# Optimization experiments

Hardware: AMD Instinct MI355X
Metric: run time of the kernel (lower is better)

Reference implementation:

```python
import jax, jax.numpy as jnp
import numpy as np

N_NODES = 100000
N_EDGES = 1600000
IN_CH = 512
HID_CH = 256
OUT_CH = 32
K = 10


def setup_inputs() -> dict:
    key = jax.random.key(0)
    k_x, k_e, k_w1, k_b1, k_w2, k_b2 = jax.random.split(key, 6)
    x = jax.random.normal(k_x, (N_NODES, IN_CH), dtype=jnp.float32)
    edge_index = jax.random.randint(k_e, (2, N_EDGES), 0, N_NODES, dtype=jnp.int64)
    s1 = 1.0 / np.sqrt(IN_CH)
    s2 = 1.0 / np.sqrt(HID_CH)
    W1 = jax.random.uniform(k_w1, (IN_CH, HID_CH), jnp.float32, -s1, s1)
    b1 = jax.random.uniform(k_b1, (HID_CH,), jnp.float32, -s1, s1)
    W2 = jax.random.uniform(k_w2, (HID_CH, OUT_CH), jnp.float32, -s2, s2)
    b2 = jax.random.uniform(k_b2, (OUT_CH,), jnp.float32, -s2, s2)
    gamma = jnp.ones((K + 1,), jnp.float32) / (K + 1)
    return {"x": x, "edge_index": edge_index, "W1": W1, "b1": b1,
            "W2": W2, "b2": b2, "gamma": gamma}


def reference(x, edge_index, W1, b1, W2, b2, gamma):
    # MLP (dropout is identity in eval mode)
    h = jax.nn.relu(x @ W1 + b1) @ W2 + b2  # [N, out]
    row, col = edge_index[0], edge_index[1]
    # symmetric normalization: deg over destination nodes (col)
    deg = jax.ops.segment_sum(jnp.ones((N_EDGES,), h.dtype), col,
                              num_segments=N_NODES)
    deg_inv_sqrt = jnp.where(deg > 0, jax.lax.rsqrt(jnp.maximum(deg, 1.0)), 0.0)
    norm = (deg_inv_sqrt[row] * deg_inv_sqrt[col])[:, None]  # [E, 1]
    out = gamma[0] * h
    h_k = h
    for k in range(1, K + 1):
        # one hop: gather source feats, scale, scatter-add to destinations
        h_k = jax.ops.segment_sum(norm * h_k[row], col, num_segments=N_NODES)
        out = out + gamma[k] * h_k
    return out
```

## Files before the change

### kernel.cpp

```cpp
#include <hip/hip_runtime.h>
#include <hip/hip_bf16.h>

#define NN    100000
#define NE    1600000
#define INCH  512
#define HIDCH 256
#define OUTCH 32
#define KHOPS 10
#define NEPAD (NE + 3 * NN)
#define NBKT  8
#define BDIV  12500
#define BCAP  204800
#define EPB_A 8192
#define EPB_B 2048

typedef __attribute__((ext_vector_type(8))) short short8;
typedef __attribute__((ext_vector_type(4))) float f32x4;

#define GLOAD_LDS16(gsrc, ldst) \
  __builtin_amdgcn_global_load_lds((const __attribute__((address_space(1))) void*)(gsrc), \
                                   (__attribute__((address_space(3))) void*)(ldst), 16, 0, 0)

constexpr size_t ws_align(size_t x) { return (x + 255) & ~(size_t)255; }
constexpr size_t USZ = ws_align((size_t)(NN + 1) * 32 * 2);
constexpr size_t USH = USZ / 2;
constexpr size_t OFF_H1    = 0;
constexpr size_t OFF_U0    = OFF_H1    + ws_align((size_t)NN*HIDCH*2);
constexpr size_t OFF_W1TH  = OFF_U0    + 11 * USZ;
constexpr size_t OFF_W1TL  = OFF_W1TH  + ws_align((size_t)HIDCH*INCH*2);
constexpr size_t OFF_W2TH  = OFF_W1TL  + ws_align((size_t)HIDCH*INCH*2);
constexpr size_t OFF_W2TL  = OFF_W2TH  + ws_align((size_t)OUTCH*HIDCH*2);
constexpr size_t OFF_DEG   = OFF_W2TL  + ws_align((size_t)OUTCH*HIDCH*2);
constexpr size_t OFF_DIS   = OFF_DEG   + ws_align((size_t)NN*4);
constexpr size_t OFF_RP    = OFF_DIS   + ws_align((size_t)NN*4);
constexpr size_t OFF_CUR   = OFF_RP    + ws_align((size_t)(NN+1)*4);
constexpr size_t OFF_NAP   = OFF_CUR   + ws_align((size_t)NN*4);
constexpr size_t OFF_POSV  = OFF_NAP   + ws_align((size_t)NN*4);
constexpr size_t OFF_PDGP  = OFF_POSV  + ws_align((size_t)NN*4);
constexpr size_t OFF_D2P   = OFF_PDGP  + ws_align((size_t)NN*4);
constexpr size_t OFF_DSQP  = OFF_D2P   + ws_align((size_t)NN*4);
constexpr size_t OFF_CSR   = OFF_DSQP  + ws_align((size_t)NN*4);
constexpr size_t OFF_PART  = OFF_CSR   + ws_align((size_t)NEPAD*4);
constexpr size_t OFF_OFFS  = OFF_PART  + ws_align(512);
constexpr size_t OFF_BCNT  = OFF_OFFS  + ws_align(512);
constexpr size_t OFF_BINH  = OFF_BCNT  + ws_align(32);
constexpr size_t OFF_BINO  = OFF_BINH  + ws_align(256);
constexpr size_t OFF_BINC  = OFF_BINO  + ws_align(256);
constexpr size_t OFF_EPK8  = OFF_BINC  + ws_align(256);

__device__ __forceinline__ unsigned short bf16_rne(float f) {
  unsigned int u = __float_as_uint(f);
  u += 0x7fffu + ((u >> 16) & 1u);
  return (unsigned short)(u >> 16);
}
__device__ __forceinline__ float bf16_to_f32(unsigned short h) {
  return __uint_as_float(((unsigned int)h) << 16);
}
__device__ __forceinline__ float bflo(unsigned int w) {
  return __uint_as_float(w << 16);
}
__device__ __forceinline__ float bfhi(unsigned int w) {
  return __uint_as_float(w & 0xffff0000u);
}

__global__ __launch_bounds__(256) void k_bucket(const int* __restrict__ ei,
                                                int* __restrict__ deg,
                                                int* __restrict__ bcnt,
                                                int2* __restrict__ epk8) {
  __shared__ int hist[NBKT], rbase[NBKT], lcur[NBKT];
  const int t = threadIdx.x;
  const int e0 = blockIdx.x * EPB_A;
  if (t < NBKT) hist[t] = 0;
  __syncthreads();
  for (int i = t; i < EPB_A; i += 256) {
    int e = e0 + i;
    if (e < NE) {
      int c = ei[NE + e];
      atomicAdd(&deg[c], 1);
      atomicAdd(&hist[c / BDIV], 1);
    }
  }
  __syncthreads();
  if (t < NBKT) {
    rbase[t] = atomicAdd(&bcnt[t], hist[t]);
    lcur[t] = 0;
  }
  __syncthreads();
  for (int i = t; i < EPB_A; i += 256) {
    int e = e0 + i;
    if (e < NE) {
      int r = ei[e], c = ei[NE + e];
      int b = c / BDIV;
      int slot = atomicAdd(&lcur[b], 1);
      epk8[(size_t)b * BCAP + rbase[b] + slot] = make_int2(r, c);
    }
  }
}

__global__ __launch_bounds__(256) void k_dis(const int* __restrict__ deg,
                                             float* __restrict__ dis,
                                             unsigned short* __restrict__ u0) {
  int v = blockIdx.x * 256 + threadIdx.x;
  if (v < NN) {
    int d = deg[v];
    dis[v] = d > 0 ? rsqrtf((float)d) : 0.0f;
  }
  if (blockIdx.x == 0 && threadIdx.x < 160) {
    int tab = threadIdx.x >> 4, li = threadIdx.x & 15;
    ((unsigned int*)(u0 + (size_t)tab * USH))[(size_t)NN * 16 + li] = 0;
  }
}

__global__ __launch_bounds__(256) void k_hist(const int* __restrict__ deg,
                                              int* __restrict__ binh) {
  __shared__ int h[64];
  const int t = threadIdx.x;
  if (t < 64) h[t] = 0;
  __syncthreads();
  int v = blockIdx.x * 256 + t;
  if (v < NN) {
    int bin = ((deg[v] + 3) & ~3) >> 2;
    if (bin > 63) bin = 63;
    atomicAdd(&h[bin], 1);
  }
  __syncthreads();
  if (t < 64 && h[t]) atomicAdd(&binh[t], h[t]);
}

__global__ __launch_bounds__(64) void k_binscan(const int* __restrict__ binh,
                                                int* __restrict__ bino,
                                                int* __restrict__ binc) {
  __shared__ int s[64];
  int t = threadIdx.x;
  int v = binh[t];
  s[t] = v;
  __syncthreads();
  for (int d = 1; d < 64; d <<= 1) {
    int x = (t >= d) ? s[t - d] : 0;
    __syncthreads();
    s[t] += x;
    __syncthreads();
  }
  bino[t] = s[t] - v;
  binc[t] = s[t] - v;
}

__global__ __launch_bounds__(256) void k_place(const int* __restrict__ deg,
                                               int* __restrict__ binc,
                                               int* __restrict__ nap,
                                               int* __restrict__ posv,
                                               int* __restrict__ pdgp) {
  __shared__ int h[64], rb[64], lc[64];
  const int t = threadIdx.x;
  if (t < 64) h[t] = 0;
  __syncthreads();
  int v = blockIdx.x * 256 + t;
  int pdeg = 0, bin = 0;
  bool valid = v < NN;
  if (valid) {
    pdeg = (deg[v] + 3) & ~3;
    bin = pdeg >> 2;
    if (bin > 63) bin = 63;
    atomicAdd(&h[bin], 1);
  }
  __syncthreads();
  if (t < 64) {
    rb[t] = h[t] ? atomicAdd(&binc[t], h[t]) : 0;
    lc[t] = 0;
  }
  __syncthreads();
  if (valid) {
    int slot = atomicAdd(&lc[bin], 1);
    int pos = rb[bin] + slot;
    nap[pos] = v;
    posv[v] = pos;
    pdgp[pos] = pdeg;
  }
}

__global__ __launch_bounds__(256) void k_scan1(const int* __restrict__ pdgp,
                                               int* __restrict__ rp,
                                               int* __restrict__ part) {
  __shared__ int s[256];
  int b = blockIdx.x, t = threadIdx.x;
  int base = b * 1024 + t * 4;
  int v0 = (base + 0 < NN) ? pdgp[base + 0] : 0;
  int v1 = (base + 1 < NN) ? pdgp[base + 1] : 0;
  int v2 = (base + 2 < NN) ? pdgp[base + 2] : 0;
  int v3 = (base + 3 < NN) ? pdgp[base + 3] : 0;
  int tot = v0 + v1 + v2 + v3;
  s[t] = tot;
  __syncthreads();
  for (int d = 1; d < 256; d <<= 1) {
    int x = (t >= d) ? s[t - d] : 0;
    __syncthreads();
    s[t] += x;
    __syncthreads();
  }
  int excl = s[t] - tot;
  if (t == 255) part[b] = s[255];
  if (base + 0 < NN) rp[base + 0] = excl;
  if (base + 1 < NN) rp[base + 1] = excl + v0;
  if (base + 2 < NN) rp[base + 2] = excl + v0 + v1;
  if (base + 3 < NN) rp[base + 3] = excl + v0 + v1 + v2;
}

__global__ __launch_bounds__(128) void k_scan2(const int* __restrict__ part,
                                               int* __restrict__ offs) {
  __shared__ int s[128];
  int t = threadIdx.x;
  int v = (t < 98) ? part[t] : 0;
  s[t] = v;
  __syncthreads();
  for (int d = 1; d < 128; d <<= 1) {
    int x = (t >= d) ? s[t - d] : 0;
    __syncthreads();
    s[t] += x;
    __syncthreads();
  }
  if (t < 98) offs[t] = s[t] - v;
}

__global__ __launch_bounds__(256) void k_scan3(int* __restrict__ rp,
                                               const int* __restrict__ offs,
                                               const int* __restrict__ part) {
  int b = blockIdx.x, t = threadIdx.x;
  int o = offs[b];
  int base = b * 1024 + t * 4;
#pragma unroll
  for (int j = 0; j < 4; ++j) {
    int i = base + j;
    if (i < NN) rp[i] += o;
  }
  if (b == 0 && t == 0) rp[NN] = offs[97] + part[97];
}

__global__ __launch_bounds__(256) void k_curinit(const int* __restrict__ nap,
                                                 const int* __restrict__ rp,
                                                 const int* __restrict__ deg,
                                                 const float* __restrict__ dis,
                                                 int* __restrict__ cur,
                                                 float* __restrict__ d2p,
                                                 float* __restrict__ dsqp) {
  int p = blockIdx.x * 256 + threadIdx.x;
  if (p < NN) {
    int v = nap[p];
    cur[v] = rp[p];
    float dv = dis[v];
    d2p[p] = dv * dv;
    int d = deg[v];
    dsqp[p] = d > 0 ? sqrtf((float)d) : 0.0f;
  }
}

__global__ __launch_bounds__(256) void k_fill2(const int2* __restrict__ epk8,
                                               const int* __restrict__ bcnt,
                                               const int* __restrict__ posv,
                                               int* __restrict__ cur,
                                               int* __restrict__ csrc) {
  const int bucket = blockIdx.x & 7;
  const int chunk = blockIdx.x >> 3;
  const int cnt = bcnt[bucket];
  const int lo = chunk * EPB_B;
  int n = cnt - lo;
  if (n > EPB_B) n = EPB_B;
  const int2* src = epk8 + (size_t)bucket * BCAP + lo;
  for (int i = threadIdx.x; i < n; i += 256) {
    int2 rc = src[i];
    int p = atomicAdd(&cur[rc.y], 1);
    csrc[p] = posv[rc.x];
  }
}

__global__ __launch_bounds__(256) void k_pad(const int* __restrict__ nap,
                                             const int* __restrict__ cur,
                                             const int* __restrict__ rp,
                                             int* __restrict__ csrc) {
  int p = blockIdx.x * 256 + threadIdx.x;
  if (p < NN) {
    int v = nap[p];
    int q = cur[v], e = rp[p + 1];
    for (; q < e; ++q) csrc[q] = NN;
  }
}

__global__ __launch_bounds__(256) void k_splitT(const float* __restrict__ src,
                                                unsigned short* __restrict__ dh,
                                                unsigned short* __restrict__ dl,
                                                int K, int N) {
  int idx = blockIdx.x * 256 + threadIdx.x;
  if (idx >= K * N) return;
  int n = idx / K, k = idx - n * K;
  float v = src[(size_t)k * N + n];
  unsigned short h = bf16_rne(v);
  dh[idx] = h;
  dl[idx] = bf16_rne(v - bf16_to_f32(h));
}

__global__ __launch_bounds__(512, 2) void k_gemm1(const float* __restrict__ X,
                                                  const unsigned short* __restrict__ W1Th,
                                                  const float* __restrict__ bias1,
                                                  unsigned short* __restrict__ H1bf) {
  __shared__ __align__(16) unsigned short Ah[2][4096];
  __shared__ __align__(16) unsigned short Bh[2][8192];
  const int t = threadIdx.x;
  const int m0 = blockIdx.x * 128;
  const int w = t >> 6, lane = t & 63;
  const int wm = w >> 2, wn = w & 3;

  const int arow = t >> 2;
  const int achk = t & 3;
  int axrow = m0 + arow; if (axrow >= NN) axrow = NN - 1;
  const float* aptr = X + (size_t)axrow * INCH + achk * 8;
  int aidx = (arow >> 4) * 512 + ((arow & 15) + achk * 16) * 8;
  aidx ^= ((aidx >> 7) & 3) << 4;
  const int aroff = (lane * 8) ^ (((lane >> 4) & 3) << 4);

  const int bn0 = (w * 16) + (lane & 15);
  const int bko = (lane >> 4) * 8;
  const unsigned short* bs0 = W1Th + (size_t)bn0 * INCH + bko;
  const unsigned short* bs1 = W1Th + (size_t)(bn0 + 128) * INCH + bko;

  f32x4 acc[4][4] = {};
  float4 av0, av1;

  av0 = *(const float4*)(aptr);
  av1 = *(const float4*)(aptr + 4);
  GLOAD_LDS16(bs0, &Bh[0][w * 512]);
  GLOAD_LDS16(bs1, &Bh[0][(w + 8) * 512]);
  {
    float af[8] = {av0.x, av0.y, av0.z, av0.w, av1.x, av1.y, av1.z, av1.w};
    short8 ah;
#pragma unroll
    for (int i = 0; i < 8; ++i) {
      unsigned int u = __float_as_uint(af[i]);
      ah[i] = (short)((u + 0x7fffu + ((u >> 16) & 1u)) >> 16);
    }
    *(short8*)&Ah[0][aidx] = ah;
  }
  __syncthreads();

#pragma unroll
  for (int it = 0; it < 16; ++it) {
    const int cur = it & 1, nxt = cur ^ 1;
    const int k0 = it * 32;
    if (it < 15) {
      av0 = *(const float4*)(aptr + k0 + 32);
      av1 = *(const float4*)(aptr + k0 + 36);
      GLOAD_LDS16(bs0 + k0 + 32, &Bh[nxt][w * 512]);
      GLOAD_LDS16(bs1 + k0 + 32, &Bh[nxt][(w + 8) * 512]);
    }
    short8 afrag[4];
#pragma unroll
    for (int mf = 0; mf < 4; ++mf)
      afrag[mf] = *(const short8*)&Ah[cur][(wm * 4 + mf) * 512 + aroff];
#pragma unroll
    for (int nf = 0; nf < 4; ++nf) {
      short8 bfh = *(const short8*)&Bh[cur][(wn * 4 + nf) * 512 + lane * 8];
#pragma unroll
      for (int mf = 0; mf < 4; ++mf) {
        acc[mf][nf] = __builtin_amdgcn_mfma_f32_16x16x32_bf16(afrag[mf], bfh, acc[mf][nf], 0, 0, 0);
      }
    }
    if (it < 15) {
      float af[8] = {av0.x, av0.y, av0.z, av0.w, av1.x, av1.y, av1.z, av1.w};
      short8 ah;
#pragma unroll
      for (int i = 0; i < 8; ++i) {
        unsigned int u = __float_as_uint(af[i]);
        ah[i] = (short)((u + 0x7fffu + ((u >> 16) & 1u)) >> 16);
      }
      *(short8*)&Ah[nxt][aidx] = ah;
    }
    __syncthreads();
  }

  const int colbase = wn * 64 + (lane & 15);
  const int rowbase = m0 + wm * 64 + ((lane >> 4) << 2);
#pragma unroll
  for (int nf = 0; nf < 4; ++nf) {
    int col = colbase + nf * 16;
    float b = bias1[col];
#pragma unroll
    for (int mf = 0; mf < 4; ++mf) {
#pragma unroll
      for (int r = 0; r < 4; ++r) {
        int row = rowbase + mf * 16 + r;
        if (row < NN) {
          float h = fmaxf(acc[mf][nf][r] + b, 0.f);
          H1bf[(size_t)row * HIDCH + col] = bf16_rne(h);
        }
      }
    }
  }
}

__global__ __launch_bounds__(256) void k_gemm2(const unsigned short* __restrict__ H1bf,
                                               const unsigned short* __restrict__ W2Th,
                                               const unsigned short* __restrict__ W2Tl,
                                               const float* __restrict__ bias2,
                                               const float* __restrict__ gamma,
                                               const float* __restrict__ dis,
                                               const int* __restrict__ posv,
                                               unsigned short* __restrict__ u0,
                                               float* __restrict__ out) {
  __shared__ __align__(16) unsigned short A2[8192];
  __shared__ __align__(16) unsigned short B2h[2048], B2l[2048];
  const int t = threadIdx.x;
  const int m0 = blockIdx.x * 128;

  const int arow = t >> 1;
  int axrow = m0 + arow; if (axrow >= NN) axrow = NN - 1;
  const int akb = (t & 1) * 32;
  const unsigned short* ap = H1bf + (size_t)axrow * HIDCH + akb;
  const int abase = ((arow >> 4) * 2 + (akb >> 5)) * 512 + (arow & 15) * 8;

  const int bnr = t >> 3, bkq = (t & 7) * 8;
  const int bslot = ((bnr >> 4) * 2 + (bkq >> 5)) * 512 +
                    ((bnr & 15) + (((bkq & 31) >> 3) << 4)) * 8;
  const unsigned short* bhp = W2Th + (size_t)bnr * HIDCH + bkq;
  const unsigned short* blp = W2Tl + (size_t)bnr * HIDCH + bkq;

  const int w = t >> 6, lane = t & 63;

  f32x4 acc[2][2] = {};

  for (int k0 = 0; k0 < HIDCH; k0 += 64) {
    uint4 a0 = *(const uint4*)(ap + k0);
    uint4 a1 = *(const uint4*)(ap + k0 + 8);
    uint4 a2 = *(const uint4*)(ap + k0 + 16);
    uint4 a3 = *(const uint4*)(ap + k0 + 24);
    uint4 bh = *(const uint4*)(bhp + k0);
    uint4 bl = *(const uint4*)(blp + k0);

    __syncthreads();

    *(uint4*)&A2[abase + 0 * 128] = a0;
    *(uint4*)&A2[abase + 1 * 128] = a1;
    *(uint4*)&A2[abase + 2 * 128] = a2;
    *(uint4*)&A2[abase + 3 * 128] = a3;
    *(uint4*)&B2h[bslot] = bh;
    *(uint4*)&B2l[bslot] = bl;

    __syncthreads();

    const short8* AV  = (const short8*)A2;
    const short8* BHV = (const short8*)B2h;
    const short8* BLV = (const short8*)B2l;
#pragma unroll
    for (int k32 = 0; k32 < 2; ++k32) {
      short8 bfh[2], bfl[2];
#pragma unroll
      for (int nf = 0; nf < 2; ++nf) {
        bfh[nf] = BHV[(nf * 2 + k32) * 64 + lane];
        bfl[nf] = BLV[(nf * 2 + k32) * 64 + lane];
      }
#pragma unroll
      for (int mf = 0; mf < 2; ++mf) {
        short8 a = AV[((w * 2 + mf) * 2 + k32) * 64 + lane];
#pragma unroll
        for (int nf = 0; nf < 2; ++nf) {
          acc[mf][nf] = __builtin_amdgcn_mfma_f32_16x16x32_bf16(a, bfh[nf], acc[mf][nf], 0, 0, 0);
          acc[mf][nf] = __builtin_amdgcn_mfma_f32_16x16x32_bf16(a, bfl[nf], acc[mf][nf], 0, 0, 0);
        }
      }
    }
  }

  const float g0 = gamma[0];
  const int colb = lane & 15;
  const int rowb = m0 + w * 32 + ((lane >> 4) << 2);
  const float b2c0 = bias2[colb], b2c1 = bias2[16 + colb];
#pragma unroll
  for (int mf = 0; mf < 2; ++mf) {
#pragma unroll
    for (int r = 0; r < 4; ++r) {
      int row = rowb + mf * 16 + r;
      if (row < NN) {
        float dv = dis[row];
        float h0 = acc[mf][0][r] + b2c0;
        float h1 = acc[mf][1][r] + b2c1;
        size_t op = (size_t)posv[row] * 32 + colb;
        u0[op] = bf16_rne(dv * h0);
        u0[op + 16] = bf16_rne(dv * h1);
        size_t o = (size_t)row * 32 + colb;
        out[o] = g0 * h0;
        out[o + 16] = g0 * h1;
      }
    }
  }
}

__global__ __launch_bounds__(256) void k_hop(const unsigned short* __restrict__ Uin,
                                             unsigned short* __restrict__ Uout,
                                             const int* __restrict__ rp,
                                             const int* __restrict__ csrc,
                                             const float* __restrict__ d2p) {
  const int t = threadIdx.x;
  const int g = t >> 4;
  const int li = t & 15;
  const int p = blockIdx.x * 16 + g;
  const int s = rp[p], e = rp[p + 1];
  const unsigned int* Uin32 = (const unsigned int*)Uin;

  float ax0 = 0.f, ay0 = 0.f, ax1 = 0.f, ay1 = 0.f;
  float ax2 = 0.f, ay2 = 0.f, ax3 = 0.f, ay3 = 0.f;
  int j = s;
  for (; j + 8 <= e; j += 8) {
    int4 sa = *(const int4*)&csrc[j];
    int4 sb = *(const int4*)&csrc[j + 4];
    unsigned int w0 = Uin32[(size_t)sa.x * 16 + li];
    unsigned int w1 = Uin32[(size_t)sa.y * 16 + li];
    unsigned int w2 = Uin32[(size_t)sa.z * 16 + li];
    unsigned int w3 = Uin32[(size_t)sa.w * 16 + li];
    unsigned int w4 = Uin32[(size_t)sb.x * 16 + li];
    unsigned int w5 = Uin32[(size_t)sb.y * 16 + li];
    unsigned int w6 = Uin32[(size_t)sb.z * 16 + li];
    unsigned int w7 = Uin32[(size_t)sb.w * 16 + li];
    ax0 += bflo(w0); ay0 += bfhi(w0);
    ax1 += bflo(w1); ay1 += bfhi(w1);
    ax2 += bflo(w2); ay2 += bfhi(w2);
    ax3 += bflo(w3); ay3 += bfhi(w3);
    ax0 += bflo(w4); ay0 += bfhi(w4);
    ax1 += bflo(w5); ay1 += bfhi(w5);
    ax2 += bflo(w6); ay2 += bfhi(w6);
    ax3 += bflo(w7); ay3 += bfhi(w7);
  }
  if (j < e) {
    int4 sa = *(const int4*)&csrc[j];
    unsigned int w0 = Uin32[(size_t)sa.x * 16 + li];
    unsigned int w1 = Uin32[(size_t)sa.y * 16 + li];
    unsigned int w2 = Uin32[(size_t)sa.z * 16 + li];
    unsigned int w3 = Uin32[(size_t)sa.w * 16 + li];
    ax0 += bflo(w0); ay0 += bfhi(w0);
    ax1 += bflo(w1); ay1 += bfhi(w1);
    ax2 += bflo(w2); ay2 += bfhi(w2);
    ax3 += bflo(w3); ay3 += bfhi(w3);
  }
  const float Sx = (ax0 + ax1) + (ax2 + ax3);
  const float Sy = (ay0 + ay1) + (ay2 + ay3);
  const float d2 = d2p[p];
  unsigned int packed = (unsigned int)bf16_rne(d2 * Sx) |
                        ((unsigned int)bf16_rne(d2 * Sy) << 16);
  ((unsigned int*)Uout)[(size_t)p * 16 + li] = packed;
}

__global__ __launch_bounds__(256) void k_merge(const unsigned short* __restrict__ u1,
                                               const int* __restrict__ nap,
                                               const float* __restrict__ dsqp,
                                               const float* __restrict__ gamma,
                                               float* __restrict__ out) {
  const int idx = blockIdx.x * 256 + threadIdx.x;
  const int p = idx >> 4;
  const int li = idx & 15;
  const int v = nap[p];
  const float f = dsqp[p];
  const size_t o = (size_t)v * 32 + li * 2;
  float2 acc = *(const float2*)&out[o];
#pragma unroll
  for (int k = 0; k < KHOPS; ++k) {
    unsigned int w = ((const unsigned int*)(u1 + (size_t)k * USH))[(size_t)p * 16 + li];
    float gk = gamma[k + 1] * f;
    acc.x = fmaf(gk, bflo(w), acc.x);
    acc.y = fmaf(gk, bfhi(w), acc.y);
  }
  *(float2*)&out[o] = acc;
}

extern "C" void kernel_launch(void* const* d_in, const int* in_sizes, int n_in,
                              void* d_out, int out_size, void* d_ws, size_t ws_size,
                              hipStream_t stream) {
  const float* x     = (const float*)d_in[0];
  const int*   ei    = (const int*)d_in[1];
  const float* W1    = (const float*)d_in[2];
  const float* b1    = (const float*)d_in[3];
  const float* W2    = (const float*)d_in[4];
  const float* b2    = (const float*)d_in[5];
  const float* gamma = (const float*)d_in[6];
  float* out = (float*)d_out;

  char* ws = (char*)d_ws;
  unsigned short* h1bf = (unsigned short*)(ws + OFF_H1);
  unsigned short* u0   = (unsigned short*)(ws + OFF_U0);
  unsigned short* w1th = (unsigned short*)(ws + OFF_W1TH);
  unsigned short* w1tl = (unsigned short*)(ws + OFF_W1TL);
  unsigned short* w2th = (unsigned short*)(ws + OFF_W2TH);
  unsigned short* w2tl = (unsigned short*)(ws + OFF_W2TL);
  int*   deg  = (int*)(ws + OFF_DEG);
  float* dis  = (float*)(ws + OFF_DIS);
  int*   rp   = (int*)(ws + OFF_RP);
  int*   cur  = (int*)(ws + OFF_CUR);
  int*   nap  = (int*)(ws + OFF_NAP);
  int*   posv = (int*)(ws + OFF_POSV);
  int*   pdgp = (int*)(ws + OFF_PDGP);
  float* d2p  = (float*)(ws + OFF_D2P);
  float* dsqp = (float*)(ws + OFF_DSQP);
  int*   csrc = (int*)(ws + OFF_CSR);
  int*   part = (int*)(ws + OFF_PART);
  int*   offs = (int*)(ws + OFF_OFFS);
  int*   bcnt = (int*)(ws + OFF_BCNT);
  int*   binh = (int*)(ws + OFF_BINH);
  int*   bino = (int*)(ws + OFF_BINO);
  int*   binc = (int*)(ws + OFF_BINC);
  int2*  epk8 = (int2*)(ws + OFF_EPK8);

  hipMemsetAsync(deg, 0, NN * sizeof(int), stream);
  hipMemsetAsync(bcnt, 0, NBKT * sizeof(int), stream);
  hipMemsetAsync(binh, 0, 64 * sizeof(int), stream);

  k_splitT<<<(INCH * HIDCH + 255) / 256, 256, 0, stream>>>(W1, w1th, w1tl, INCH, HIDCH);
  k_splitT<<<(HIDCH * OUTCH + 255) / 256, 256, 0, stream>>>(W2, w2th, w2tl, HIDCH, OUTCH);

  k_bucket<<<(NE + EPB_A - 1) / EPB_A, 256, 0, stream>>>(ei, deg, bcnt, epk8);
  k_dis<<<(NN + 255) / 256, 256, 0, stream>>>(deg, dis, u0);
  k_hist<<<(NN + 255) / 256, 256, 0, stream>>>(deg, binh);
  k_binscan<<<1, 64, 0, stream>>>(binh, bino, binc);
  k_place<<<(NN + 255) / 256, 256, 0, stream>>>(deg, binc, nap, posv, pdgp);
  k_scan1<<<98, 256, 0, stream>>>(pdgp, rp, part);
  k_scan2<<<1, 128, 0, stream>>>(part, offs);
  k_scan3<<<98, 256, 0, stream>>>(rp, offs, part);
  k_curinit<<<(NN + 255) / 256, 256, 0, stream>>>(nap, rp, deg, dis, cur, d2p, dsqp);
  k_fill2<<<(BCAP / EPB_B) * NBKT, 256, 0, stream>>>(epk8, bcnt, posv, cur, csrc);
  k_pad<<<(NN + 255) / 256, 256, 0, stream>>>(nap, cur, rp, csrc);

  k_gemm1<<<(NN + 127) / 128, 512, 0, stream>>>(x, w1th, b1, h1bf);
  k_gemm2<<<(NN + 127) / 128, 256, 0, stream>>>(h1bf, w2th, w2tl, b2, gamma, dis,
                                                posv, u0, out);

  for (int k = 1; k <= KHOPS; ++k) {
    unsigned short* uin  = u0 + (size_t)(k - 1) * USH;
    unsigned short* uout = u0 + (size_t)k * USH;
    k_hop<<<NN / 16, 256, 0, stream>>>(uin, uout, rp, csrc, d2p);
  }

  k_merge<<<NN * 16 / 256, 256, 0, stream>>>(u0 + USH, nap, dsqp, gamma, out);
}
```

Before: 523.7 us.

## Fuse second GEMM into first GEMM epilogue and merge degree histogram into k_dis

```diff
diff --git a/kernel.cpp b/kernel.cpp
--- a/kernel.cpp
+++ b/kernel.cpp
@@ -24,8 +24,7 @@
 constexpr size_t ws_align(size_t x) { return (x + 255) & ~(size_t)255; }
 constexpr size_t USZ = ws_align((size_t)(NN + 1) * 32 * 2);
 constexpr size_t USH = USZ / 2;
-constexpr size_t OFF_H1    = 0;
-constexpr size_t OFF_U0    = OFF_H1    + ws_align((size_t)NN*HIDCH*2);
+constexpr size_t OFF_U0    = 0;
 constexpr size_t OFF_W1TH  = OFF_U0    + 11 * USZ;
 constexpr size_t OFF_W1TL  = OFF_W1TH  + ws_align((size_t)HIDCH*INCH*2);
 constexpr size_t OFF_W2TH  = OFF_W1TL  + ws_align((size_t)HIDCH*INCH*2);
@@ -99,32 +98,26 @@
 
 __global__ __launch_bounds__(256) void k_dis(const int* __restrict__ deg,
                                              float* __restrict__ dis,
-                                             unsigned short* __restrict__ u0) {
-  int v = blockIdx.x * 256 + threadIdx.x;
+                                             unsigned short* __restrict__ u0,
+                                             int* __restrict__ binh) {
+  __shared__ int h[64];
+  const int t = threadIdx.x;
+  if (t < 64) h[t] = 0;
+  __syncthreads();
+  int v = blockIdx.x * 256 + t;
   if (v < NN) {
     int d = deg[v];
     dis[v] = d > 0 ? rsqrtf((float)d) : 0.0f;
-  }
-  if (blockIdx.x == 0 && threadIdx.x < 160) {
-    int tab = threadIdx.x >> 4, li = threadIdx.x & 15;
-    ((unsigned int*)(u0 + (size_t)tab * USH))[(size_t)NN * 16 + li] = 0;
-  }
-}
-
-__global__ __launch_bounds__(256) void k_hist(const int* __restrict__ deg,
-                                              int* __restrict__ binh) {
-  __shared__ int h[64];
-  const int t = threadIdx.x;
-  if (t < 64) h[t] = 0;
-  __syncthreads();
-  int v = blockIdx.x * 256 + t;
-  if (v < NN) {
-    int bin = ((deg[v] + 3) & ~3) >> 2;
+    int bin = ((d + 3) & ~3) >> 2;
     if (bin > 63) bin = 63;
     atomicAdd(&h[bin], 1);
   }
   __syncthreads();
   if (t < 64 && h[t]) atomicAdd(&binh[t], h[t]);
+  if (blockIdx.x == 0 && t < 160) {
+    int tab = t >> 4, li = t & 15;
+    ((unsigned int*)(u0 + (size_t)tab * USH))[(size_t)NN * 16 + li] = 0;
+  }
 }
 
 __global__ __launch_bounds__(64) void k_binscan(const int* __restrict__ binh,
@@ -297,10 +290,16 @@
   dl[idx] = bf16_rne(v - bf16_to_f32(h));
 }
 
-__global__ __launch_bounds__(512, 2) void k_gemm1(const float* __restrict__ X,
-                                                  const unsigned short* __restrict__ W1Th,
-                                                  const float* __restrict__ bias1,
-                                                  unsigned short* __restrict__ H1bf) {
+__global__ __launch_bounds__(512, 2) void k_mlp(const float* __restrict__ X,
+                                                const unsigned short* __restrict__ W1Th,
+                                                const float* __restrict__ bias1,
+                                                const unsigned short* __restrict__ W2Th,
+                                                const float* __restrict__ bias2,
+                                                const float* __restrict__ gamma,
+                                                const float* __restrict__ dis,
+                                                const int* __restrict__ posv,
+                                                unsigned short* __restrict__ u0,
+                                                float* __restrict__ out) {
   __shared__ __align__(16) unsigned short Ah[2][4096];
   __shared__ __align__(16) unsigned short Bh[2][8192];
   const int t = threadIdx.x;
@@ -375,117 +374,97 @@
     __syncthreads();
   }
 
-  const int colbase = wn * 64 + (lane & 15);
-  const int rowbase = m0 + wm * 64 + ((lane >> 4) << 2);
-#pragma unroll
-  for (int nf = 0; nf < 4; ++nf) {
-    int col = colbase + nf * 16;
-    float b = bias1[col];
-#pragma unroll
-    for (int mf = 0; mf < 4; ++mf) {
-#pragma unroll
-      for (int r = 0; r < 4; ++r) {
-        int row = rowbase + mf * 16 + r;
-        if (row < NN) {
-          float h = fmaxf(acc[mf][nf][r] + b, 0.f);
-          H1bf[(size_t)row * HIDCH + col] = bf16_rne(h);
+  unsigned short* AhF = &Ah[0][0];
+  unsigned short* BhF = &Bh[0][0];
+
+  {
+#pragma unroll
+    for (int q = 0; q < 2; ++q) {
+      int u = w * 2 + q;
+      int ngrp = u >> 3, k32 = u & 7;
+      const unsigned short* src = W2Th + (size_t)(ngrp * 16 + (lane & 15)) * HIDCH
+                                       + k32 * 32 + (lane >> 4) * 8;
+      GLOAD_LDS16(src, &AhF[u * 512]);
+    }
+  }
+
+  const int row15b = (lane >> 4) << 2;
+  const int kcol = lane & 15;
+  float bset[4];
+#pragma unroll
+  for (int nf = 0; nf < 4; ++nf) bset[nf] = bias1[wn * 64 + nf * 16 + kcol];
+
+  if (wn < 2) {
+    const int kbase = wn * 64;
+#pragma unroll
+    for (int nf = 0; nf < 4; ++nf) {
+      int kh = kbase + nf * 16 + kcol;
+      int base = ((wm * 4) * 4 + (kh >> 5)) * 512 + ((kh >> 3) & 3) * 128 + (kh & 7);
+#pragma unroll
+      for (int mf = 0; mf < 4; ++mf) {
+#pragma unroll
+        for (int r = 0; r < 4; ++r) {
+          float h = fmaxf(acc[mf][nf][r] + bset[nf], 0.f);
+          BhF[base + mf * 2048 + (row15b + r) * 8] = bf16_rne(h);
         }
       }
     }
   }
-}
-
-__global__ __launch_bounds__(256) void k_gemm2(const unsigned short* __restrict__ H1bf,
-                                               const unsigned short* __restrict__ W2Th,
-                                               const unsigned short* __restrict__ W2Tl,
-                                               const float* __restrict__ bias2,
-                                               const float* __restrict__ gamma,
-                                               const float* __restrict__ dis,
-                                               const int* __restrict__ posv,
-                                               unsigned short* __restrict__ u0,
-                                               float* __restrict__ out) {
-  __shared__ __align__(16) unsigned short A2[8192];
-  __shared__ __align__(16) unsigned short B2h[2048], B2l[2048];
-  const int t = threadIdx.x;
-  const int m0 = blockIdx.x * 128;
-
-  const int arow = t >> 1;
-  int axrow = m0 + arow; if (axrow >= NN) axrow = NN - 1;
-  const int akb = (t & 1) * 32;
-  const unsigned short* ap = H1bf + (size_t)axrow * HIDCH + akb;
-  const int abase = ((arow >> 4) * 2 + (akb >> 5)) * 512 + (arow & 15) * 8;
-
-  const int bnr = t >> 3, bkq = (t & 7) * 8;
-  const int bslot = ((bnr >> 4) * 2 + (bkq >> 5)) * 512 +
-                    ((bnr & 15) + (((bkq & 31) >> 3) << 4)) * 8;
-  const unsigned short* bhp = W2Th + (size_t)bnr * HIDCH + bkq;
-  const unsigned short* blp = W2Tl + (size_t)bnr * HIDCH + bkq;
-
-  const int w = t >> 6, lane = t & 63;
-
-  f32x4 acc[2][2] = {};
-
-  for (int k0 = 0; k0 < HIDCH; k0 += 64) {
-    uint4 a0 = *(const uint4*)(ap + k0);
-    uint4 a1 = *(const uint4*)(ap + k0 + 8);
-    uint4 a2 = *(const uint4*)(ap + k0 + 16);
-    uint4 a3 = *(const uint4*)(ap + k0 + 24);
-    uint4 bh = *(const uint4*)(bhp + k0);
-    uint4 bl = *(const uint4*)(blp + k0);
-
-    __syncthreads();
-
-    *(uint4*)&A2[abase + 0 * 128] = a0;
-    *(uint4*)&A2[abase + 1 * 128] = a1;
-    *(uint4*)&A2[abase + 2 * 128] = a2;
-    *(uint4*)&A2[abase + 3 * 128] = a3;
-    *(uint4*)&B2h[bslot] = bh;
-    *(uint4*)&B2l[bslot] = bl;
-
-    __syncthreads();
-
-    const short8* AV  = (const short8*)A2;
-    const short8* BHV = (const short8*)B2h;
-    const short8* BLV = (const short8*)B2l;
-#pragma unroll
-    for (int k32 = 0; k32 < 2; ++k32) {
-      short8 bfh[2], bfl[2];
-#pragma unroll
-      for (int nf = 0; nf < 2; ++nf) {
-        bfh[nf] = BHV[(nf * 2 + k32) * 64 + lane];
-        bfl[nf] = BLV[(nf * 2 + k32) * 64 + lane];
-      }
-#pragma unroll
-      for (int mf = 0; mf < 2; ++mf) {
-        short8 a = AV[((w * 2 + mf) * 2 + k32) * 64 + lane];
-#pragma unroll
-        for (int nf = 0; nf < 2; ++nf) {
-          acc[mf][nf] = __builtin_amdgcn_mfma_f32_16x16x32_bf16(a, bfh[nf], acc[mf][nf], 0, 0, 0);
-          acc[mf][nf] = __builtin_amdgcn_mfma_f32_16x16x32_bf16(a, bfl[nf], acc[mf][nf], 0, 0, 0);
+  __syncthreads();
+
+  f32x4 acc2[2] = {};
+#pragma unroll
+  for (int s = 0; s < 4; ++s) {
+    short8 a2 = *(const short8*)&BhF[(w * 4 + s) * 512 + lane * 8];
+#pragma unroll
+    for (int nf = 0; nf < 2; ++nf) {
+      short8 bf = *(const short8*)&AhF[(nf * 8 + s) * 512 + lane * 8];
+      acc2[nf] = __builtin_amdgcn_mfma_f32_16x16x32_bf16(a2, bf, acc2[nf], 0, 0, 0);
+    }
+  }
+  __syncthreads();
+
+  if (wn >= 2) {
+    const int kbase = (wn - 2) * 64;
+#pragma unroll
+    for (int nf = 0; nf < 4; ++nf) {
+      int kh = kbase + nf * 16 + kcol;
+      int base = ((wm * 4) * 4 + (kh >> 5)) * 512 + ((kh >> 3) & 3) * 128 + (kh & 7);
+#pragma unroll
+      for (int mf = 0; mf < 4; ++mf) {
+#pragma unroll
+        for (int r = 0; r < 4; ++r) {
+          float h = fmaxf(acc[mf][nf][r] + bset[nf], 0.f);
+          BhF[base + mf * 2048 + (row15b + r) * 8] = bf16_rne(h);
         }
       }
     }
   }
+  __syncthreads();
+
+#pragma unroll
+  for (int s = 0; s < 4; ++s) {
+    short8 a2 = *(const short8*)&BhF[(w * 4 + s) * 512 + lane * 8];
+#pragma unroll
+    for (int nf = 0; nf < 2; ++nf) {
+      short8 bf = *(const short8*)&AhF[(nf * 8 + 4 + s) * 512 + lane * 8];
+      acc2[nf] = __builtin_amdgcn_mfma_f32_16x16x32_bf16(a2, bf, acc2[nf], 0, 0, 0);
+    }
+  }
 
   const float g0 = gamma[0];
-  const int colb = lane & 15;
-  const int rowb = m0 + w * 32 + ((lane >> 4) << 2);
-  const float b2c0 = bias2[colb], b2c1 = bias2[16 + colb];
-#pragma unroll
-  for (int mf = 0; mf < 2; ++mf) {
+  const float b2c[2] = {bias2[kcol], bias2[16 + kcol]};
+#pragma unroll
+  for (int nf = 0; nf < 2; ++nf) {
 #pragma unroll
     for (int r = 0; r < 4; ++r) {
-      int row = rowb + mf * 16 + r;
+      int row = m0 + w * 16 + row15b + r;
       if (row < NN) {
+        float h = acc2[nf][r] + b2c[nf];
         float dv = dis[row];
-        float h0 = acc[mf][0][r] + b2c0;
-        float h1 = acc[mf][1][r] + b2c1;
-        size_t op = (size_t)posv[row] * 32 + colb;
-        u0[op] = bf16_rne(dv * h0);
-        u0[op + 16] = bf16_rne(dv * h1);
-        size_t o = (size_t)row * 32 + colb;
-        out[o] = g0 * h0;
-        out[o + 16] = g0 * h1;
+        size_t op = (size_t)posv[row] * 32 + nf * 16 + kcol;
+        u0[op] = bf16_rne(dv * h);
+        out[(size_t)row * 32 + nf * 16 + kcol] = g0 * h;
       }
     }
   }
@@ -580,7 +559,6 @@
   float* out = (float*)d_out;
 
   char* ws = (char*)d_ws;
-  unsigned short* h1bf = (unsigned short*)(ws + OFF_H1);
   unsigned short* u0   = (unsigned short*)(ws + OFF_U0);
   unsigned short* w1th = (unsigned short*)(ws + OFF_W1TH);
   unsigned short* w1tl = (unsigned short*)(ws + OFF_W1TL);
@@ -612,8 +590,7 @@
   k_splitT<<<(HIDCH * OUTCH + 255) / 256, 256, 0, stream>>>(W2, w2th, w2tl, HIDCH, OUTCH);
 
   k_bucket<<<(NE + EPB_A - 1) / EPB_A, 256, 0, stream>>>(ei, deg, bcnt, epk8);
-  k_dis<<<(NN + 255) / 256, 256, 0, stream>>>(deg, dis, u0);
-  k_hist<<<(NN + 255) / 256, 256, 0, stream>>>(deg, binh);
+  k_dis<<<(NN + 255) / 256, 256, 0, stream>>>(deg, dis, u0, binh);
   k_binscan<<<1, 64, 0, stream>>>(binh, bino, binc);
   k_place<<<(NN + 255) / 256, 256, 0, stream>>>(deg, binc, nap, posv, pdgp);
   k_scan1<<<98, 256, 0, stream>>>(pdgp, rp, part);
@@ -623,9 +600,8 @@
   k_fill2<<<(BCAP / EPB_B) * NBKT, 256, 0, stream>>>(epk8, bcnt, posv, cur, csrc);
   k_pad<<<(NN + 255) / 256, 256, 0, stream>>>(nap, cur, rp, csrc);
 
-  k_gemm1<<<(NN + 127) / 128, 512, 0, stream>>>(x, w1th, b1, h1bf);
-  k_gemm2<<<(NN + 127) / 128, 256, 0, stream>>>(h1bf, w2th, w2tl, b2, gamma, dis,
-                                                posv, u0, out);
+  k_mlp<<<(NN + 127) / 128, 512, 0, stream>>>(x, w1th, b1, w2th, b2, gamma, dis,
+                                              posv, u0, out);
 
   for (int k = 1; k <= KHOPS; ++k) {
     unsigned short* uin  = u0 + (size_t)(k - 1) * USH;
```

Result: faster. 511.7 us (-2.3%).
